# Performance work log

Measured on AMD Instinct MI355X. Metric: run time of the kernel, lower is better.

The kernel has to match this reference:

```python
import jax, jax.numpy as jnp
import numpy as np

B, S, H = 4, 2048, 1024
NH, HD = 16, 64
LN_EPS = 1e-5


def _l2norm(x, axis=-1, eps=1e-12):
    n = jnp.sqrt(jnp.sum(x * x, axis=axis, keepdims=True))
    return x / jnp.maximum(n, eps)


def setup_inputs() -> dict:
    key = jax.random.key(0)
    ks = jax.random.split(key, 10)
    sd = 0.02
    x = jax.random.normal(ks[0], (B, S, H), jnp.float32)
    Wq = jax.random.normal(ks[1], (H, H), jnp.float32) * sd
    Wk = jax.random.normal(ks[2], (H, H), jnp.float32) * sd
    Wv = jax.random.normal(ks[3], (H, H), jnp.float32) * sd
    Wa = jax.random.normal(ks[4], (NH, H), jnp.float32) * sd
    ba = jnp.zeros((NH,), jnp.float32)
    Wb = jax.random.normal(ks[5], (NH, H), jnp.float32) * sd
    bb = jnp.zeros((NH,), jnp.float32)
    Wg = jax.random.normal(ks[6], (H, H), jnp.float32) * sd
    Wo = jax.random.normal(ks[7], (H, H), jnp.float32) * sd
    ln_g = jnp.ones((H,), jnp.float32)
    ln_b = jnp.zeros((H,), jnp.float32)
    return {"x": x, "Wq": Wq, "Wk": Wk, "Wv": Wv, "Wa": Wa, "ba": ba,
            "Wb": Wb, "bb": bb, "Wg": Wg, "Wo": Wo, "ln_g": ln_g, "ln_b": ln_b}


def _forward(x, Wq, Wk, Wv, Wa, ba, Wb, bb, Wg, Wo, ln_g, ln_b):
    q = _l2norm((x @ Wq.T).reshape(B, S, NH, HD))  # [B,S,nh,hd]
    k = _l2norm((x @ Wk.T).reshape(B, S, NH, HD))
    v = jax.nn.silu(x @ Wv.T).reshape(B, S, NH, HD)
    alpha = jax.nn.sigmoid(x @ Wa.T + ba)  # [B,S,nh]
    beta = jax.nn.sigmoid(x @ Wb.T + bb)   # [B,S,nh]

    def step(state, inp):
        a_t, b_t, k_t, v_t, q_t = inp  # a,b: [B,nh]; k,v,q: [B,nh,hd]
        a_ = a_t[:, :, None, None]
        b_ = b_t[:, :, None, None]
        kk = k_t[..., :, None] * k_t[..., None, :]  # [B,nh,hd,hd]
        state = a_ * state * (1.0 - b_ * kk) + b_ * (v_t[..., :, None] * k_t[..., None, :])
        out_t = jnp.sum(state * q_t[..., None, :], axis=-1)  # [B,nh,hd]
        return state, out_t

    # time-major xs for scan
    xs = (jnp.moveaxis(alpha, 1, 0), jnp.moveaxis(beta, 1, 0),
          jnp.moveaxis(k, 1, 0), jnp.moveaxis(v, 1, 0), jnp.moveaxis(q, 1, 0))
    state0 = jnp.zeros((B, NH, HD, HD), x.dtype)
    _, outs = jax.lax.scan(step, state0, xs)  # [S,B,nh,hd]
    out = jnp.moveaxis(outs, 0, 1).reshape(B, S, H)

    # LayerNorm over total_dim
    mu = jnp.mean(out, axis=-1, keepdims=True)
    var = jnp.var(out, axis=-1, keepdims=True)
    out = (out - mu) / jnp.sqrt(var + LN_EPS) * ln_g + ln_b

    out = out * jax.nn.silu(x @ Wg.T)
    return out @ Wo.T


def reference(x, Wq, Wk, Wv, Wa, ba, Wb, bb, Wg, Wo, ln_g, ln_b):
    return _forward(x, Wq, Wk, Wv, Wa, ba, Wb, bb, Wg, Wo, ln_g, ln_b)
```

## Files before the change

kernel.cpp:

```cpp
#include <hip/hip_runtime.h>

typedef unsigned short u16;
typedef __bf16 bf16x8 __attribute__((ext_vector_type(8)));
typedef float f32x4 __attribute__((ext_vector_type(4)));

constexpr int Bq  = 4;
constexpr int Sq  = 2048;
constexpr int Hq  = 1024;
constexpr int NHq = 16;
constexpr int HDq = 64;
constexpr int CCH = 16;
constexpr int LCH = 128;

constexpr size_t OFF_WB = 0;
constexpr size_t OFF_XB = 10485760;
constexpr size_t OFF_Q  = 27262976;
constexpr size_t OFF_K  = 60817408;
constexpr size_t OFF_V  = 94371840;
constexpr size_t OFF_G  = 127926272;
constexpr size_t OFF_AL = 161480704;
constexpr size_t OFF_BE = 162004992;
constexpr size_t OFF_P  = 162529280;
constexpr size_t OFF_O  = 179306496;

__device__ __forceinline__ u16 f2bf(float f) {
  unsigned u = __float_as_uint(f);
  u += 0x7fffu + ((u >> 16) & 1u);
  return (u16)(u >> 16);
}
__device__ __forceinline__ float sigmoidf_(float x) { return 1.f / (1.f + __expf(-x)); }

__device__ __forceinline__ void async16(const void* g, void* l) {
  __builtin_amdgcn_global_load_lds((const __attribute__((address_space(1))) void*)g,
                                   (__attribute__((address_space(3))) void*)l, 16, 0, 0);
}

__global__ __launch_bounds__(256) void cvt_x_kernel(const float* __restrict__ in, u16* __restrict__ outp) {
  const size_t i = ((size_t)blockIdx.x * 256 + threadIdx.x) * 4;
  float4 f = *(const float4*)(in + i);
  ushort4 u; u.x = f2bf(f.x); u.y = f2bf(f.y); u.z = f2bf(f.z); u.w = f2bf(f.w);
  *(ushort4*)(outp + i) = u;
}

__global__ __launch_bounds__(256) void cvt_w_kernel(const float* __restrict__ w0, const float* __restrict__ w1,
    const float* __restrict__ w2, const float* __restrict__ w3, const float* __restrict__ w4,
    u16* __restrict__ outp) {
  const int z = blockIdx.z;
  const float* src = (z == 0) ? w0 : (z == 1) ? w1 : (z == 2) ? w2 : (z == 3) ? w3 : w4;
  const size_t i = ((size_t)blockIdx.x * 256 + threadIdx.x) * 4;
  float4 f = *(const float4*)(src + i);
  ushort4 u; u.x = f2bf(f.x); u.y = f2bf(f.y); u.z = f2bf(f.z); u.w = f2bf(f.w);
  *(ushort4*)(outp + (size_t)z * (1024 * 1024) + i) = u;
}

__global__ __launch_bounds__(256) void cvt_ab_kernel(const float* __restrict__ Wa, const float* __restrict__ Wb,
    u16* __restrict__ outp) {
  const size_t i = ((size_t)blockIdx.x * 256 + threadIdx.x) * 4;
  const int row = (int)(i >> 10);
  ushort4 u;
  if (row < 32) {
    const float* src = (row < 16) ? (Wa + i) : (Wb + i - 16 * 1024);
    float4 f = *(const float4*)src;
    u.x = f2bf(f.x); u.y = f2bf(f.y); u.z = f2bf(f.z); u.w = f2bf(f.w);
  } else {
    u.x = u.y = u.z = u.w = 0;
  }
  *(ushort4*)(outp + i) = u;
}

__global__ __launch_bounds__(256) void gemm_bt(const u16* __restrict__ A, const u16* __restrict__ Wall,
    const u16* __restrict__ Wab,
    float* __restrict__ Cq, float* __restrict__ Ck, float* __restrict__ Cv, float* __restrict__ Cg,
    float* __restrict__ al, float* __restrict__ be,
    const float* __restrict__ ba, const float* __restrict__ bb, int mode) {
  constexpr int GK = 1024, GN = 1024;
  const int z = blockIdx.z;
  if (mode == 1 && z == 4 && blockIdx.y > 0) return;
  __shared__ __align__(16) u16 As[128 * 32];
  __shared__ __align__(16) u16 Bs[128 * 32];
  const int tid = threadIdx.x;
  const int w = tid >> 6, lane = tid & 63;
  const int m0 = blockIdx.x * 128, n0 = blockIdx.y * 128;
  const u16* W = (mode == 1 && z == 4) ? Wab : (Wall + (size_t)z * (1024 * 1024));
  const int rrow = lane >> 2;
  const int kc8 = (lane & 3) * 8;
  const u16* gA = A + (size_t)(m0 + w * 32 + rrow) * GK + kc8;
  const u16* gB = W + (size_t)(n0 + w * 32 + rrow) * GK + kc8;
  u16* lA = As + (w * 32) * 32;
  u16* lB = Bs + (w * 32) * 32;
  const int qd = lane >> 4, l15 = lane & 15;
  const int wm = (w >> 1) * 64, wn = (w & 1) * 64;
  f32x4 acc[4][4] = {};
  for (int kt = 0; kt < GK; kt += 32) {
    async16(gA,           lA);
    async16(gA + 16 * GK, lA + 16 * 32);
    async16(gB,           lB);
    async16(gB + 16 * GK, lB + 16 * 32);
    gA += 32; gB += 32;
    __syncthreads();
    bf16x8 af[4], bfr[4];
    #pragma unroll
    for (int i = 0; i < 4; ++i) {
      af[i]  = *(const bf16x8*)(As + (wm + i * 16 + l15) * 32 + qd * 8);
      bfr[i] = *(const bf16x8*)(Bs + (wn + i * 16 + l15) * 32 + qd * 8);
    }
    #pragma unroll
    for (int i = 0; i < 4; ++i)
      #pragma unroll
      for (int j = 0; j < 4; ++j)
        acc[i][j] = __builtin_amdgcn_mfma_f32_16x16x32_bf16(af[i], bfr[j], acc[i][j], 0, 0, 0);
    __syncthreads();
  }
  if (mode == 1 && z == 4) {
    if (wn == 0) {
      const float bav = ba[l15], bbv = bb[l15];
      #pragma unroll
      for (int i = 0; i < 4; ++i) {
        const int row = m0 + wm + i * 16 + qd * 4;
        #pragma unroll
        for (int r = 0; r < 4; ++r) {
          al[(size_t)(row + r) * 16 + l15] = sigmoidf_(acc[i][0][r] + bav);
          be[(size_t)(row + r) * 16 + l15] = sigmoidf_(acc[i][1][r] + bbv);
        }
      }
    }
    return;
  }
  if (mode == 1 && (z == 0 || z == 1)) {
    #pragma unroll
    for (int i = 0; i < 4; ++i)
      #pragma unroll
      for (int r = 0; r < 4; ++r) {
        float ss = acc[i][0][r] * acc[i][0][r] + acc[i][1][r] * acc[i][1][r]
                 + acc[i][2][r] * acc[i][2][r] + acc[i][3][r] * acc[i][3][r];
        ss += __shfl_xor(ss, 1); ss += __shfl_xor(ss, 2);
        ss += __shfl_xor(ss, 4); ss += __shfl_xor(ss, 8);
        const float rn = 1.f / fmaxf(sqrtf(ss), 1e-12f);
        acc[i][0][r] *= rn; acc[i][1][r] *= rn; acc[i][2][r] *= rn; acc[i][3][r] *= rn;
      }
  } else if (mode == 1 && z == 2) {
    #pragma unroll
    for (int i = 0; i < 4; ++i)
      #pragma unroll
      for (int j = 0; j < 4; ++j)
        #pragma unroll
        for (int r = 0; r < 4; ++r)
          acc[i][j][r] = acc[i][j][r] * sigmoidf_(acc[i][j][r]);
  }
  float* C = (mode == 0) ? Cq : ((z == 0) ? Cq : (z == 1) ? Ck : (z == 2) ? Cv : Cg);
  #pragma unroll
  for (int i = 0; i < 4; ++i) {
    const int row = m0 + wm + i * 16 + qd * 4;
    #pragma unroll
    for (int j = 0; j < 4; ++j) {
      const int col = n0 + wn + j * 16 + l15;
      #pragma unroll
      for (int r = 0; r < 4; ++r)
        C[(size_t)(row + r) * GN + col] = acc[i][j][r];
    }
  }
}

struct ScanLds1 { float kb[2][2][16 * 64]; float vb[2][2][16 * 64]; float ab[2][2][32]; };
struct ScanLds2 { float kb[2][2][16 * 64]; float qb[2][2][16 * 64]; float vb[2][2][16 * 64]; float ab[2][2][32]; };

__global__ __launch_bounds__(256, 2) void scan_p1(const float* __restrict__ k, const float* __restrict__ v,
    const float* __restrict__ al, const float* __restrict__ be,
    float* __restrict__ P, float* __restrict__ Q) {
  __shared__ ScanLds1 L;
  const int tid = threadIdx.x, wv = tid >> 6, lane = tid & 63;
  const int bh = blockIdx.x >> 3, cp = blockIdx.x & 7;
  const int b = bh >> 4, h = bh & 15;
  const int cw = wv >> 1, half = wv & 1;
  const int c = cp * 2 + cw;
  const int rg = lane >> 3, cg = lane & 7;
  const int r0 = half * 32 + rg * 4, c8 = cg * 8;
  const size_t base0[2] = { ((size_t)(b * Sq + (cp * 2 + 0) * LCH)) * 1024 + h * 64,
                            ((size_t)(b * Sq + (cp * 2 + 1) * LCH)) * 1024 + h * 64 };
  const size_t ab0[2]   = { ((size_t)(b * Sq + (cp * 2 + 0) * LCH)) * 16 + h,
                            ((size_t)(b * Sq + (cp * 2 + 1) * LCH)) * 16 + h };
  const int tokw = lane >> 4, seg = lane & 15;
  auto stage = [&](int tile, int bi) {
    #pragma unroll
    for (int j = 0; j < 4; ++j) {
      const int job = wv * 4 + j;
      const int ch = job >> 3, rem = job & 7, arr = rem >> 2, i = rem & 3;
      const float* src = arr ? v : k;
      float* dst = arr ? &L.vb[bi][ch][i * 256] : &L.kb[bi][ch][i * 256];
      async16(src + base0[ch] + (size_t)(tile * 16 + i * 4 + tokw) * 1024 + seg * 4, dst);
    }
    if (wv == 0) {
      const int ch = lane >> 5, w16 = (lane >> 4) & 1, tt = lane & 15;
      const float* s = w16 ? be : al;
      L.ab[bi][ch][w16 * 16 + tt] = s[ab0[ch] + (size_t)(tile * 16 + tt) * 16];
    }
  };
  float Pr[32], Qr[32];
  #pragma unroll
  for (int i = 0; i < 32; ++i) { Pr[i] = 1.f; Qr[i] = 0.f; }
  stage(0, 0);
  for (int tile = 0; tile < 8; ++tile) {
    __syncthreads();
    if (tile < 7) stage(tile + 1, (tile + 1) & 1);
    const int bi = tile & 1;
    const float* kbp = L.kb[bi][cw];
    const float* vbp = L.vb[bi][cw];
    const float* abp = L.ab[bi][cw];
    #pragma unroll 2
    for (int tt = 0; tt < 16; ++tt) {
      const float a = abp[tt], bt = abp[16 + tt];
      float4 kcv0 = *(const float4*)(kbp + tt * 64 + c8);
      float4 kcv1 = *(const float4*)(kbp + tt * 64 + c8 + 4);
      float4 krvv = *(const float4*)(kbp + tt * 64 + r0);
      float4 vrvv = *(const float4*)(vbp + tt * 64 + r0);
      const float kcv[8] = {kcv0.x, kcv0.y, kcv0.z, kcv0.w, kcv1.x, kcv1.y, kcv1.z, kcv1.w};
      const float krv[4] = {krvv.x, krvv.y, krvv.z, krvv.w};
      const float vrv[4] = {vrvv.x, vrvv.y, vrvv.z, vrvv.w};
      const float abt = a * bt;
      float c1[4], c2[4];
      #pragma unroll
      for (int i = 0; i < 4; ++i) { c1[i] = abt * krv[i]; c2[i] = bt * vrv[i]; }
      #pragma unroll
      for (int i = 0; i < 4; ++i)
        #pragma unroll
        for (int j = 0; j < 8; ++j) {
          const int e = i * 8 + j;
          const float A = fmaf(-c1[i], kcv[j], a);
          Qr[e] = fmaf(A, Qr[e], c2[i] * kcv[j]);
          Pr[e] *= A;
        }
    }
  }
  const size_t pbase = ((size_t)bh * CCH + c) * 4096 + (size_t)c8;
  #pragma unroll
  for (int i = 0; i < 4; ++i) {
    const size_t pi = pbase + (size_t)(r0 + i) * 64;
    *(float4*)(P + pi) = make_float4(Pr[i*8],   Pr[i*8+1], Pr[i*8+2], Pr[i*8+3]);
    *(float4*)(P + pi + 4) = make_float4(Pr[i*8+4], Pr[i*8+5], Pr[i*8+6], Pr[i*8+7]);
    *(float4*)(Q + pi) = make_float4(Qr[i*8],   Qr[i*8+1], Qr[i*8+2], Qr[i*8+3]);
    *(float4*)(Q + pi + 4) = make_float4(Qr[i*8+4], Qr[i*8+5], Qr[i*8+6], Qr[i*8+7]);
  }
}

__global__ __launch_bounds__(256) void scan_comb(float* __restrict__ P, const float* __restrict__ Q) {
  const int g = blockIdx.x * 256 + threadIdx.x;
  const int elem = g & 4095;
  const int bh = g >> 12;
  float s = 0.f;
  for (int c = 0; c < CCH; ++c) {
    const size_t idx = ((size_t)bh * CCH + c) * 4096 + elem;
    const float p = P[idx], qq = Q[idx];
    P[idx] = s;
    s = fmaf(p, s, qq);
  }
}

__global__ __launch_bounds__(256, 2) void scan_p2(const float* __restrict__ q, const float* __restrict__ k,
    const float* __restrict__ v, const float* __restrict__ al, const float* __restrict__ be,
    const float* __restrict__ Pini, float* __restrict__ o) {
  __shared__ ScanLds2 L;
  const int tid = threadIdx.x, wv = tid >> 6, lane = tid & 63;
  const int bh = blockIdx.x >> 3, cp = blockIdx.x & 7;
  const int b = bh >> 4, h = bh & 15;
  const int cw = wv >> 1, half = wv & 1;
  const int c = cp * 2 + cw;
  const int rg = lane >> 3, cg = lane & 7;
  const int r0 = half * 32 + rg * 4, c8 = cg * 8;
  const size_t base0[2] = { ((size_t)(b * Sq + (cp * 2 + 0) * LCH)) * 1024 + h * 64,
                            ((size_t)(b * Sq + (cp * 2 + 1) * LCH)) * 1024 + h * 64 };
  const size_t ab0[2]   = { ((size_t)(b * Sq + (cp * 2 + 0) * LCH)) * 16 + h,
                            ((size_t)(b * Sq + (cp * 2 + 1) * LCH)) * 16 + h };
  const size_t mybase = base0[cw];
  const size_t pbase = ((size_t)bh * CCH + c) * 4096 + (size_t)c8;
  const int tokw = lane >> 4, seg = lane & 15;
  auto stage = [&](int tile, int bi) {
    #pragma unroll
    for (int j = 0; j < 6; ++j) {
      const int job = wv * 6 + j;
      const int ch = job / 12, rem = job % 12, arr = rem >> 2, i = rem & 3;
      const float* src = (arr == 0) ? k : (arr == 1) ? q : v;
      float* dst = (arr == 0) ? &L.kb[bi][ch][i * 256] : (arr == 1) ? &L.qb[bi][ch][i * 256]
                                                                    : &L.vb[bi][ch][i * 256];
      async16(src + base0[ch] + (size_t)(tile * 16 + i * 4 + tokw) * 1024 + seg * 4, dst);
    }
    if (wv == 0) {
      const int ch = lane >> 5, w16 = (lane >> 4) & 1, tt = lane & 15;
      const float* s = w16 ? be : al;
      L.ab[bi][ch][w16 * 16 + tt] = s[ab0[ch] + (size_t)(tile * 16 + tt) * 16];
    }
  };
  float st[32];
  #pragma unroll
  for (int i = 0; i < 4; ++i) {
    float4 s0 = *(const float4*)(Pini + pbase + (size_t)(r0 + i) * 64);
    float4 s1 = *(const float4*)(Pini + pbase + (size_t)(r0 + i) * 64 + 4);
    st[i*8]   = s0.x; st[i*8+1] = s0.y; st[i*8+2] = s0.z; st[i*8+3] = s0.w;
    st[i*8+4] = s1.x; st[i*8+5] = s1.y; st[i*8+6] = s1.z; st[i*8+7] = s1.w;
  }
  stage(0, 0);
  const bool hi4 = (cg & 4), hi2 = (cg & 2);
  const int rowIdx = r0 + (cg >> 1);
  const bool doStore = ((cg & 1) == 0);
  for (int tile = 0; tile < 8; ++tile) {
    __syncthreads();
    if (tile < 7) stage(tile + 1, (tile + 1) & 1);
    const int bi = tile & 1;
    const float* kbp = L.kb[bi][cw];
    const float* qbp = L.qb[bi][cw];
    const float* vbp = L.vb[bi][cw];
    const float* abp = L.ab[bi][cw];
    #pragma unroll 2
    for (int tt = 0; tt < 16; ++tt) {
      const int t = tile * 16 + tt;
      const float a = abp[tt], bt = abp[16 + tt];
      float4 kcv0 = *(const float4*)(kbp + tt * 64 + c8);
      float4 kcv1 = *(const float4*)(kbp + tt * 64 + c8 + 4);
      float4 qcv0 = *(const float4*)(qbp + tt * 64 + c8);
      float4 qcv1 = *(const float4*)(qbp + tt * 64 + c8 + 4);
      float4 krvv = *(const float4*)(kbp + tt * 64 + r0);
      float4 vrvv = *(const float4*)(vbp + tt * 64 + r0);
      const float kcv[8] = {kcv0.x, kcv0.y, kcv0.z, kcv0.w, kcv1.x, kcv1.y, kcv1.z, kcv1.w};
      const float qcv[8] = {qcv0.x, qcv0.y, qcv0.z, qcv0.w, qcv1.x, qcv1.y, qcv1.z, qcv1.w};
      const float krv[4] = {krvv.x, krvv.y, krvv.z, krvv.w};
      const float vrv[4] = {vrvv.x, vrvv.y, vrvv.z, vrvv.w};
      const float abt = a * bt;
      float c1[4], c2[4];
      #pragma unroll
      for (int i = 0; i < 4; ++i) { c1[i] = abt * krv[i]; c2[i] = bt * vrv[i]; }
      float p[4];
      #pragma unroll
      for (int i = 0; i < 4; ++i) p[i] = 0.f;
      #pragma unroll
      for (int i = 0; i < 4; ++i)
        #pragma unroll
        for (int j = 0; j < 8; ++j) {
          const int e = i * 8 + j;
          const float A = fmaf(-c1[i], kcv[j], a);
          st[e] = fmaf(A, st[e], c2[i] * kcv[j]);
          p[i] = fmaf(st[e], qcv[j], p[i]);
        }
      float r2[2];
      #pragma unroll
      for (int i = 0; i < 2; ++i) {
        const float send = hi4 ? p[i] : p[i + 2];
        const float recv = __shfl_xor(send, 4);
        r2[i] = (hi4 ? p[i + 2] : p[i]) + recv;
      }
      float r1;
      {
        const float send = hi2 ? r2[0] : r2[1];
        const float recv = __shfl_xor(send, 2);
        r1 = (hi2 ? r2[1] : r2[0]) + recv;
      }
      const float tot = r1 + __shfl_xor(r1, 1);
      if (doStore) o[mybase + (size_t)t * 1024 + rowIdx] = tot;
    }
  }
}

__global__ __launch_bounds__(256) void ln_gate_kernel(const float* __restrict__ o, const float* __restrict__ g,
    const float* __restrict__ ln_g, const float* __restrict__ ln_b, u16* __restrict__ y) {
  const int t = blockIdx.x, tid = threadIdx.x;
  const size_t row = (size_t)t * 1024;
  float4 xv = *(const float4*)(o + row + tid * 4);
  float s  = xv.x + xv.y + xv.z + xv.w;
  float s2 = xv.x * xv.x + xv.y * xv.y + xv.z * xv.z + xv.w * xv.w;
  #pragma unroll
  for (int m = 1; m < 64; m <<= 1) { s += __shfl_xor(s, m); s2 += __shfl_xor(s2, m); }
  __shared__ float red[8];
  const int w = tid >> 6, lane = tid & 63;
  if (lane == 0) { red[w] = s; red[4 + w] = s2; }
  __syncthreads();
  s  = red[0] + red[1] + red[2] + red[3];
  s2 = red[4] + red[5] + red[6] + red[7];
  const float mu = s * (1.f / 1024.f);
  const float var = s2 * (1.f / 1024.f) - mu * mu;
  const float rstd = rsqrtf(var + 1e-5f);
  float4 gv = *(const float4*)(g + row + tid * 4);
  float4 lg = *(const float4*)(ln_g + tid * 4);
  float4 lb = *(const float4*)(ln_b + tid * 4);
  ushort4 u;
  u.x = f2bf(((xv.x - mu) * rstd * lg.x + lb.x) * (gv.x * sigmoidf_(gv.x)));
  u.y = f2bf(((xv.y - mu) * rstd * lg.y + lb.y) * (gv.y * sigmoidf_(gv.y)));
  u.z = f2bf(((xv.z - mu) * rstd * lg.z + lb.z) * (gv.z * sigmoidf_(gv.z)));
  u.w = f2bf(((xv.w - mu) * rstd * lg.w + lb.w) * (gv.w * sigmoidf_(gv.w)));
  *(ushort4*)(y + row + tid * 4) = u;
}

extern "C" void kernel_launch(void* const* d_in, const int* in_sizes, int n_in,
                              void* d_out, int out_size, void* d_ws, size_t ws_size,
                              hipStream_t stream) {
  const float* x    = (const float*)d_in[0];
  const float* Wq   = (const float*)d_in[1];
  const float* Wk   = (const float*)d_in[2];
  const float* Wv   = (const float*)d_in[3];
  const float* Wa   = (const float*)d_in[4];
  const float* ba   = (const float*)d_in[5];
  const float* Wb   = (const float*)d_in[6];
  const float* bb   = (const float*)d_in[7];
  const float* Wg   = (const float*)d_in[8];
  const float* Wo   = (const float*)d_in[9];
  const float* ln_g = (const float*)d_in[10];
  const float* ln_b = (const float*)d_in[11];
  float* out = (float*)d_out;
  char* ws = (char*)d_ws;

  u16*   wb  = (u16*)(ws + OFF_WB);
  u16*   xb  = (u16*)(ws + OFF_XB);
  float* qf  = (float*)(ws + OFF_Q);
  float* kf  = (float*)(ws + OFF_K);
  float* vf  = (float*)(ws + OFF_V);
  float* gf  = (float*)(ws + OFF_G);
  float* al  = (float*)(ws + OFF_AL);
  float* be  = (float*)(ws + OFF_BE);
  u16*   wab = (u16*)(ws + OFF_P);
  float* Pb  = (float*)(ws + OFF_P);
  float* Qc  = (float*)(ws + OFF_XB);
  float* of  = (float*)(ws + OFF_O);
  u16*   yb  = xb;

  cvt_x_kernel<<<8192, 256, 0, stream>>>(x, xb);
  cvt_w_kernel<<<dim3(1024, 1, 5), 256, 0, stream>>>(Wq, Wk, Wv, Wg, Wo, wb);
  cvt_ab_kernel<<<128, 256, 0, stream>>>(Wa, Wb, wab);
  gemm_bt<<<dim3(64, 8, 5), 256, 0, stream>>>(xb, wb, wab, qf, kf, vf, gf, al, be, ba, bb, 1);
  scan_p1<<<512, 256, 0, stream>>>(kf, vf, al, be, Pb, Qc);
  scan_comb<<<1024, 256, 0, stream>>>(Pb, Qc);
  scan_p2<<<512, 256, 0, stream>>>(qf, kf, vf, al, be, Pb, of);
  ln_gate_kernel<<<8192, 256, 0, stream>>>(of, gf, ln_g, ln_b, yb);
  gemm_bt<<<dim3(64, 8, 1), 256, 0, stream>>>(yb, wb + (size_t)4 * 1024 * 1024, wab,
                                              out, out, out, out, al, be, ba, bb, 0);
}
```

Before: 447.1 us.

## Replace GEMM with 256x256 tile, swizzled LDS, double-buffered async pipeline

```diff
diff --git a/kernel.cpp b/kernel.cpp
--- a/kernel.cpp
+++ b/kernel.cpp
@@ -68,95 +68,177 @@
   *(ushort4*)(outp + i) = u;
 }
 
-__global__ __launch_bounds__(256) void gemm_bt(const u16* __restrict__ A, const u16* __restrict__ Wall,
+
+__device__ __forceinline__ void lda4(bf16x8 af[4][2], const u16* LA, int wr, int mh, int l15, int qd, int l7) {
+#pragma unroll
+  for (int i = 0; i < 4; ++i)
+#pragma unroll
+    for (int kk = 0; kk < 2; ++kk)
+      af[i][kk] = *(const bf16x8*)(LA + (wr * 128 + mh * 64 + i * 16 + l15) * 64 + (((kk * 4 + qd) ^ l7) * 8));
+}
+__device__ __forceinline__ void ldb2(bf16x8 bf[2][2], const u16* LB, int wc, int nh, int l15, int qd, int l7) {
+#pragma unroll
+  for (int j = 0; j < 2; ++j)
+#pragma unroll
+    for (int kk = 0; kk < 2; ++kk)
+      bf[j][kk] = *(const bf16x8*)(LB + (wc * 64 + nh * 32 + j * 16 + l15) * 64 + (((kk * 4 + qd) ^ l7) * 8));
+}
+__device__ __forceinline__ void mm16(f32x4 acc[8][4], const bf16x8 af[4][2], const bf16x8 bf[2][2], int mh, int nh) {
+#pragma unroll
+  for (int i = 0; i < 4; ++i)
+#pragma unroll
+    for (int j = 0; j < 2; ++j) {
+      f32x4 c = acc[mh * 4 + i][nh * 2 + j];
+      c = __builtin_amdgcn_mfma_f32_16x16x32_bf16(af[i][0], bf[j][0], c, 0, 0, 0);
+      c = __builtin_amdgcn_mfma_f32_16x16x32_bf16(af[i][1], bf[j][1], c, 0, 0, 0);
+      acc[mh * 4 + i][nh * 2 + j] = c;
+    }
+}
+__device__ __forceinline__ void stageH(u16* LD, int bufp, int mat, int h, const u16* gRow0, int kElem,
+                                       int rr, int sl8, int wv) {
+  const u16* s0 = gRow0 + (size_t)(h * 128 + rr) * 1024 + kElem + sl8;
+  u16* d = LD + bufp * 32768 + mat * 16384 + h * 8192 + wv * 512;
+  async16(s0, d);
+  async16(s0 + (size_t)(64 * 1024), d + 4096);
+}
+
+template<int S1, int S2, int VM>
+__device__ __forceinline__ void tile16(u16* LD, int bp, int kt,
+    const u16* gA, const u16* gB, f32x4 acc[8][4], bf16x8 af[4][2], bf16x8 bf0[2][2], bf16x8 bf1[2][2],
+    int wr, int wc, int l15, int qd, int l7, int rr, int sl8, int wv) {
+  const u16* LA = LD + bp * 32768;
+  const u16* LB = LA + 16384;
+  lda4(af, LA, wr, 0, l15, qd, l7);
+  ldb2(bf0, LB, wc, 0, l15, qd, l7);
+  if (S1) stageH(LD, bp ^ 1, 0, 0, gA, (kt + 1) * 64, rr, sl8, wv);
+  __builtin_amdgcn_s_barrier();
+  asm volatile("s_waitcnt lgkmcnt(0)" ::: "memory");
+  __builtin_amdgcn_sched_barrier(0);
+  __builtin_amdgcn_s_setprio(1);
+  mm16(acc, af, bf0, 0, 0);
+  __builtin_amdgcn_s_setprio(0);
+  __builtin_amdgcn_s_barrier();
+  ldb2(bf1, LB, wc, 1, l15, qd, l7);
+  if (S1) stageH(LD, bp ^ 1, 0, 1, gA, (kt + 1) * 64, rr, sl8, wv);
+  __builtin_amdgcn_s_barrier();
+  asm volatile("s_waitcnt lgkmcnt(0)" ::: "memory");
+  __builtin_amdgcn_sched_barrier(0);
+  __builtin_amdgcn_s_setprio(1);
+  mm16(acc, af, bf1, 0, 1);
+  __builtin_amdgcn_s_setprio(0);
+  __builtin_amdgcn_s_barrier();
+  lda4(af, LA, wr, 1, l15, qd, l7);
+  if (S2) stageH(LD, bp, 1, 0, gB, (kt + 2) * 64, rr, sl8, wv);
+  __builtin_amdgcn_s_barrier();
+  asm volatile("s_waitcnt lgkmcnt(0)" ::: "memory");
+  __builtin_amdgcn_sched_barrier(0);
+  __builtin_amdgcn_s_setprio(1);
+  mm16(acc, af, bf0, 1, 0);
+  __builtin_amdgcn_s_setprio(0);
+  __builtin_amdgcn_s_barrier();
+  if (S2) stageH(LD, bp, 1, 1, gB, (kt + 2) * 64, rr, sl8, wv);
+  __builtin_amdgcn_s_barrier();
+  __builtin_amdgcn_sched_barrier(0);
+  __builtin_amdgcn_s_setprio(1);
+  mm16(acc, af, bf1, 1, 1);
+  __builtin_amdgcn_s_setprio(0);
+  if (VM == 4) asm volatile("s_waitcnt vmcnt(4)" ::: "memory");
+  else if (VM == 0) asm volatile("s_waitcnt vmcnt(0)" ::: "memory");
+  __builtin_amdgcn_s_barrier();
+}
+
+__global__ __launch_bounds__(512, 2) void gemm256(const u16* __restrict__ A, const u16* __restrict__ Wall,
     const u16* __restrict__ Wab,
     float* __restrict__ Cq, float* __restrict__ Ck, float* __restrict__ Cv, float* __restrict__ Cg,
     float* __restrict__ al, float* __restrict__ be,
     const float* __restrict__ ba, const float* __restrict__ bb, int mode) {
-  constexpr int GK = 1024, GN = 1024;
-  const int z = blockIdx.z;
-  if (mode == 1 && z == 4 && blockIdx.y > 0) return;
-  __shared__ __align__(16) u16 As[128 * 32];
-  __shared__ __align__(16) u16 Bs[128 * 32];
+  __shared__ __align__(16) u16 Lds[65536];
+  u16* LD = &Lds[0];
   const int tid = threadIdx.x;
-  const int w = tid >> 6, lane = tid & 63;
-  const int m0 = blockIdx.x * 128, n0 = blockIdx.y * 128;
-  const u16* W = (mode == 1 && z == 4) ? Wab : (Wall + (size_t)z * (1024 * 1024));
-  const int rrow = lane >> 2;
-  const int kc8 = (lane & 3) * 8;
-  const u16* gA = A + (size_t)(m0 + w * 32 + rrow) * GK + kc8;
-  const u16* gB = W + (size_t)(n0 + w * 32 + rrow) * GK + kc8;
-  u16* lA = As + (w * 32) * 32;
-  u16* lB = Bs + (w * 32) * 32;
-  const int qd = lane >> 4, l15 = lane & 15;
-  const int wm = (w >> 1) * 64, wn = (w & 1) * 64;
-  f32x4 acc[4][4] = {};
-  for (int kt = 0; kt < GK; kt += 32) {
-    async16(gA,           lA);
-    async16(gA + 16 * GK, lA + 16 * 32);
-    async16(gB,           lB);
-    async16(gB + 16 * GK, lB + 16 * 32);
-    gA += 32; gB += 32;
-    __syncthreads();
-    bf16x8 af[4], bfr[4];
-    #pragma unroll
-    for (int i = 0; i < 4; ++i) {
-      af[i]  = *(const bf16x8*)(As + (wm + i * 16 + l15) * 32 + qd * 8);
-      bfr[i] = *(const bf16x8*)(Bs + (wn + i * 16 + l15) * 32 + qd * 8);
-    }
-    #pragma unroll
-    for (int i = 0; i < 4; ++i)
-      #pragma unroll
-      for (int j = 0; j < 4; ++j)
-        acc[i][j] = __builtin_amdgcn_mfma_f32_16x16x32_bf16(af[i], bfr[j], acc[i][j], 0, 0, 0);
-    __syncthreads();
-  }
+  const int wv = tid >> 6, lane = tid & 63;
+  const int l15 = lane & 15, qd = lane >> 4, l7 = l15 & 7;
+  const int wr = wv >> 2, wc = wv & 3;
+  const int rr = tid >> 3, sl8 = ((tid & 7) ^ (rr & 7)) * 8;
+
+  int mx, ny, z;
+  const u16* Wm;
+  if (mode == 0) { mx = blockIdx.x & 31; ny = blockIdx.x >> 5; z = 0; Wm = Wall; }
+  else if (blockIdx.x < 32) { mx = blockIdx.x; ny = 0; z = 4; Wm = Wab; }
+  else {
+    const int b = blockIdx.x - 32;
+    mx = b & 31; ny = (b >> 5) & 3; z = b >> 7;
+    Wm = Wall + (size_t)z * (1024 * 1024);
+  }
+  const int m0 = mx * 256, n0 = ny * 256;
+  const u16* gA = A + (size_t)m0 * 1024;
+  const u16* gB = Wm + (size_t)n0 * 1024;
+
+  f32x4 acc[8][4] = {};
+  bf16x8 af[4][2], bf0[2][2], bf1[2][2];
+
+  stageH(LD, 0, 0, 0, gA, 0,  rr, sl8, wv);
+  stageH(LD, 0, 0, 1, gA, 0,  rr, sl8, wv);
+  stageH(LD, 0, 1, 0, gB, 0,  rr, sl8, wv);
+  stageH(LD, 0, 1, 1, gB, 0,  rr, sl8, wv);
+  stageH(LD, 1, 1, 0, gB, 64, rr, sl8, wv);
+  stageH(LD, 1, 1, 1, gB, 64, rr, sl8, wv);
+  asm volatile("s_waitcnt vmcnt(4)" ::: "memory");
+  __builtin_amdgcn_s_barrier();
+
+#pragma unroll 1
+  for (int t2 = 0; t2 < 7; ++t2) {
+    tile16<1, 1, 4>(LD, 0, 2 * t2,     gA, gB, acc, af, bf0, bf1, wr, wc, l15, qd, l7, rr, sl8, wv);
+    tile16<1, 1, 4>(LD, 1, 2 * t2 + 1, gA, gB, acc, af, bf0, bf1, wr, wc, l15, qd, l7, rr, sl8, wv);
+  }
+  tile16<1, 0, 0>(LD, 0, 14, gA, gB, acc, af, bf0, bf1, wr, wc, l15, qd, l7, rr, sl8, wv);
+  tile16<0, 0, -1>(LD, 1, 15, gA, gB, acc, af, bf0, bf1, wr, wc, l15, qd, l7, rr, sl8, wv);
+
   if (mode == 1 && z == 4) {
-    if (wn == 0) {
+    if (wc == 0) {
       const float bav = ba[l15], bbv = bb[l15];
-      #pragma unroll
-      for (int i = 0; i < 4; ++i) {
-        const int row = m0 + wm + i * 16 + qd * 4;
-        #pragma unroll
+#pragma unroll
+      for (int mi = 0; mi < 8; ++mi) {
+        const int row = m0 + wr * 128 + mi * 16 + qd * 4;
+#pragma unroll
         for (int r = 0; r < 4; ++r) {
-          al[(size_t)(row + r) * 16 + l15] = sigmoidf_(acc[i][0][r] + bav);
-          be[(size_t)(row + r) * 16 + l15] = sigmoidf_(acc[i][1][r] + bbv);
+          al[(size_t)(row + r) * 16 + l15] = sigmoidf_(acc[mi][0][r] + bav);
+          be[(size_t)(row + r) * 16 + l15] = sigmoidf_(acc[mi][1][r] + bbv);
         }
       }
     }
     return;
   }
-  if (mode == 1 && (z == 0 || z == 1)) {
-    #pragma unroll
-    for (int i = 0; i < 4; ++i)
-      #pragma unroll
+  if (mode == 1 && z <= 1) {
+#pragma unroll
+    for (int mi = 0; mi < 8; ++mi)
+#pragma unroll
       for (int r = 0; r < 4; ++r) {
-        float ss = acc[i][0][r] * acc[i][0][r] + acc[i][1][r] * acc[i][1][r]
-                 + acc[i][2][r] * acc[i][2][r] + acc[i][3][r] * acc[i][3][r];
+        float ss = acc[mi][0][r] * acc[mi][0][r] + acc[mi][1][r] * acc[mi][1][r]
+                 + acc[mi][2][r] * acc[mi][2][r] + acc[mi][3][r] * acc[mi][3][r];
         ss += __shfl_xor(ss, 1); ss += __shfl_xor(ss, 2);
         ss += __shfl_xor(ss, 4); ss += __shfl_xor(ss, 8);
         const float rn = 1.f / fmaxf(sqrtf(ss), 1e-12f);
-        acc[i][0][r] *= rn; acc[i][1][r] *= rn; acc[i][2][r] *= rn; acc[i][3][r] *= rn;
+        acc[mi][0][r] *= rn; acc[mi][1][r] *= rn; acc[mi][2][r] *= rn; acc[mi][3][r] *= rn;
       }
   } else if (mode == 1 && z == 2) {
-    #pragma unroll
-    for (int i = 0; i < 4; ++i)
-      #pragma unroll
-      for (int j = 0; j < 4; ++j)
-        #pragma unroll
+#pragma unroll
+    for (int mi = 0; mi < 8; ++mi)
+#pragma unroll
+      for (int ni = 0; ni < 4; ++ni)
+#pragma unroll
         for (int r = 0; r < 4; ++r)
-          acc[i][j][r] = acc[i][j][r] * sigmoidf_(acc[i][j][r]);
+          acc[mi][ni][r] = acc[mi][ni][r] * sigmoidf_(acc[mi][ni][r]);
   }
   float* C = (mode == 0) ? Cq : ((z == 0) ? Cq : (z == 1) ? Ck : (z == 2) ? Cv : Cg);
-  #pragma unroll
-  for (int i = 0; i < 4; ++i) {
-    const int row = m0 + wm + i * 16 + qd * 4;
-    #pragma unroll
-    for (int j = 0; j < 4; ++j) {
-      const int col = n0 + wn + j * 16 + l15;
-      #pragma unroll
+#pragma unroll
+  for (int mi = 0; mi < 8; ++mi) {
+    const int row = m0 + wr * 128 + mi * 16 + qd * 4;
+#pragma unroll
+    for (int ni = 0; ni < 4; ++ni) {
+      const int col = n0 + wc * 64 + ni * 16 + l15;
+#pragma unroll
       for (int r = 0; r < 4; ++r)
-        C[(size_t)(row + r) * GN + col] = acc[i][j][r];
+        C[(size_t)(row + r) * 1024 + col] = acc[mi][ni][r];
     }
   }
 }
@@ -421,12 +503,12 @@
 
   cvt_x_kernel<<<8192, 256, 0, stream>>>(x, xb);
   cvt_w_kernel<<<dim3(1024, 1, 5), 256, 0, stream>>>(Wq, Wk, Wv, Wg, Wo, wb);
-  cvt_ab_kernel<<<128, 256, 0, stream>>>(Wa, Wb, wab);
-  gemm_bt<<<dim3(64, 8, 5), 256, 0, stream>>>(xb, wb, wab, qf, kf, vf, gf, al, be, ba, bb, 1);
+  cvt_ab_kernel<<<256, 256, 0, stream>>>(Wa, Wb, wab);
+  gemm256<<<544, 512, 0, stream>>>(xb, wb, wab, qf, kf, vf, gf, al, be, ba, bb, 1);
   scan_p1<<<512, 256, 0, stream>>>(kf, vf, al, be, Pb, Qc);
   scan_comb<<<1024, 256, 0, stream>>>(Pb, Qc);
   scan_p2<<<512, 256, 0, stream>>>(qf, kf, vf, al, be, Pb, of);
   ln_gate_kernel<<<8192, 256, 0, stream>>>(of, gf, ln_g, ln_b, yb);
-  gemm_bt<<<dim3(64, 8, 1), 256, 0, stream>>>(yb, wb + (size_t)4 * 1024 * 1024, wab,
-                                              out, out, out, out, al, be, ba, bb, 0);
-}
+  gemm256<<<128, 512, 0, stream>>>(yb, wb + (size_t)4 * 1024 * 1024, wab,
+                                   out, out, out, out, al, be, ba, bb, 0);
+}
```

Result: faster. 425.7 us (-4.8%).
